# Kernel optimization log

Measured on AMD Instinct MI355X. Metric: run time of the kernel, lower is better.

## Reference

```python
import jax, jax.numpy as jnp
import numpy as np

VOCAB, SEQ, D_IN, HID, N_CLS, BATCH = 50257, 128, 768, 512, 9, 256


def setup_inputs() -> dict:
    key = jax.random.key(0)
    ks = jax.random.split(key, 12)
    s = 0.02
    return {
        "input_ids": jax.random.randint(ks[0], (BATCH, SEQ), 0, VOCAB),
        "tok_emb": jax.random.normal(ks[1], (VOCAB, D_IN), jnp.float32) * s,
        "pos_emb": jax.random.normal(ks[2], (SEQ, D_IN), jnp.float32) * s,
        # stacked per-gate Linear weights, gate order (i, f, g, o); Linear stores (out, in)
        "W1": jax.random.normal(ks[3], (4, HID, D_IN), jnp.float32) * s,
        "R1": jax.random.normal(ks[4], (4, HID, HID), jnp.float32) * s,
        "b1": jax.random.normal(ks[5], (4, HID), jnp.float32) * s,
        "W2": jax.random.normal(ks[6], (4, HID, HID), jnp.float32) * s,
        "R2": jax.random.normal(ks[7], (4, HID, HID), jnp.float32) * s,
        "b2": jax.random.normal(ks[8], (4, HID), jnp.float32) * s,
        "Wo": jax.random.normal(ks[9], (N_CLS, HID), jnp.float32) * s,
        "bo": jax.random.normal(ks[10], (N_CLS,), jnp.float32) * s,
    }


def _cell(x, h, c, W, R, b):
    # all four gate linears fused into one einsum each for x and h
    g = jnp.einsum('bi,ghi->gbh', x, W) + jnp.einsum('bj,ghj->gbh', h, R) + b[:, None, :]
    i = jax.nn.sigmoid(g[0])
    f = jax.nn.sigmoid(g[1])
    m = jnp.tanh(g[2])
    o = jax.nn.sigmoid(g[3])
    c_next = m * i + f * c
    h_next = o * jnp.tanh(c_next)
    return h_next, c_next


def reference(input_ids, tok_emb, pos_emb, W1, R1, b1, W2, R2, b2, Wo, bo):
    embeds = tok_emb[input_ids] + pos_emb[None, :, :]  # (B, S, D)
    B = embeds.shape[0]
    H = R1.shape[-1]
    x_seq = jnp.swapaxes(embeds, 0, 1)  # (S, B, D)
    init = tuple(jnp.zeros((B, H), embeds.dtype) for _ in range(4))

    def step(carry, x_t):
        h1, c1, h2, c2 = carry
        h1, c1 = _cell(x_t, h1, c1, W1, R1, b1)
        h2, c2 = _cell(h1, h2, c2, W2, R2, b2)
        out = h2 @ Wo.T + bo  # (B, num_class)
        return (h1, c1, h2, c2), out

    _, outs = jax.lax.scan(step, init, x_seq)  # (S, B, C)
    return jnp.swapaxes(outs, 0, 1)  # (B, S, C)
```

## Files before the change

kernel.cpp:

```cpp
#include <hip/hip_runtime.h>
#include <hip/hip_bf16.h>
#include <stdint.h>

#define BATCH_ 256
#define SEQ_   128
#define DIN_   768
#define HID_   512
#define NG_    2048
#define NCLS_  9

typedef unsigned short u16;
typedef unsigned int u32;
typedef unsigned long long u64;
typedef __attribute__((ext_vector_type(8))) short bf16x8;
typedef __attribute__((ext_vector_type(4))) float f32x4;

__device__ __forceinline__ float bf2f(u16 u) {
  return __builtin_bit_cast(float, (uint32_t)u << 16);
}
__device__ __forceinline__ u16 f2bf(float f) {
  uint32_t x = __builtin_bit_cast(uint32_t, f);
  uint32_t r = (x + 0x7fffu + ((x >> 16) & 1u)) >> 16;
  return (u16)r;
}

__device__ __forceinline__ void gload_lds16(const void* g, void* l) {
#if defined(__has_builtin)
#if __has_builtin(__builtin_amdgcn_global_load_lds)
  __builtin_amdgcn_global_load_lds((const __attribute__((address_space(1))) void*)g,
                                   (__attribute__((address_space(3))) void*)l, 16, 0, 0);
  return;
#endif
#endif
  *(uint4*)l = *(const uint4*)g;
}

__device__ __forceinline__ u32 aload32(const u32* p) {
  return __hip_atomic_load(p, __ATOMIC_RELAXED, __HIP_MEMORY_SCOPE_AGENT);
}
__device__ __forceinline__ void astore32(u32* p, u32 v) {
  __hip_atomic_store(p, v, __ATOMIC_RELAXED, __HIP_MEMORY_SCOPE_AGENT);
}

__global__ void castk(const float* __restrict__ s, u16* __restrict__ d, int n4) {
  int i = blockIdx.x * blockDim.x + threadIdx.x;
  if (i < n4) {
    float4 v = ((const float4*)s)[i];
    ushort4 o;
    o.x = f2bf(v.x); o.y = f2bf(v.y); o.z = f2bf(v.z); o.w = f2bf(v.w);
    ((ushort4*)d)[i] = o;
  }
}

__global__ __launch_bounds__(192) void embed_k(const int* __restrict__ ids,
                                               const float* __restrict__ tok,
                                               const float* __restrict__ pos,
                                               u16* __restrict__ X) {
  const int row = blockIdx.x;
  const int t = row >> 8, b = row & 255;
  const int id = ids[b * SEQ_ + t];
  const float4* tr = (const float4*)(tok + (size_t)id * DIN_);
  const float4* pr = (const float4*)(pos + (size_t)t * DIN_);
  const int i = threadIdx.x;
  float4 v = tr[i], p = pr[i];
  ushort4 o;
  o.x = f2bf(v.x + p.x); o.y = f2bf(v.y + p.y);
  o.z = f2bf(v.z + p.z); o.w = f2bf(v.w + p.w);
  ((ushort4*)(X + (size_t)row * DIN_))[i] = o;
}

__global__ __launch_bounds__(256) void gemm_bt(const u16* __restrict__ A,
                                               const u16* __restrict__ Bm,
                                               const float* __restrict__ bias,
                                               u16* __restrict__ C,
                                               int M, int N, int K) {
  __shared__ __align__(16) u16 As[128 * 64];
  __shared__ __align__(16) u16 Bs[128 * 64];
  const int tid = threadIdx.x;
  const int lane = tid & 63;
  const int wave = tid >> 6;
  const int m0 = blockIdx.y * 128;
  const int n0 = blockIdx.x * 128;
  const int wm = (wave >> 1) * 64;
  const int wn = (wave & 1) * 64;
  const int lr = lane & 15;
  const int lg = lane >> 4;
  f32x4 acc[4][4] = {};

  for (int k0 = 0; k0 < K; k0 += 64) {
#pragma unroll
    for (int it = 0; it < 4; ++it) {
      int e = it * 256 + tid;
      int r = e >> 3, c8 = (e & 7) * 8;
      gload_lds16(A + (size_t)(m0 + r) * K + k0 + c8, &As[e * 8]);
      gload_lds16(Bm + (size_t)(n0 + r) * K + k0 + c8, &Bs[e * 8]);
    }
    __syncthreads();
#pragma unroll
    for (int kk = 0; kk < 64; kk += 32) {
      bf16x8 af[4], bfr[4];
#pragma unroll
      for (int i = 0; i < 4; ++i) {
        af[i]  = *(const bf16x8*)&As[(wm + i * 16 + lr) * 64 + kk + lg * 8];
        bfr[i] = *(const bf16x8*)&Bs[(wn + i * 16 + lr) * 64 + kk + lg * 8];
      }
#pragma unroll
      for (int i = 0; i < 4; ++i)
#pragma unroll
        for (int j = 0; j < 4; ++j)
          acc[i][j] = __builtin_amdgcn_mfma_f32_16x16x32_bf16(af[i], bfr[j], acc[i][j], 0, 0, 0);
    }
    __syncthreads();
  }
#pragma unroll
  for (int i = 0; i < 4; ++i) {
#pragma unroll
    for (int j = 0; j < 4; ++j) {
      int col = n0 + wn + j * 16 + lr;
      float bv = bias[col];
#pragma unroll
      for (int q = 0; q < 4; ++q) {
        int row = m0 + wm + i * 16 + lg * 4 + q;
        C[(size_t)row * N + col] = f2bf(acc[i][j][q] + bv);
      }
    }
  }
}

__device__ __forceinline__ void stage32r(char* dst, const u16* src, int tid) {
  const u64* s64 = (const u64*)src;
#pragma unroll
  for (int i = 0; i < 8; ++i) {
    int e = i * 512 + tid, r = e >> 7, c8 = e & 127;
    u64 v = s64[(size_t)r * 128 + c8];
    *(u64*)(dst + r * 1024 + ((((c8 >> 1) ^ (r & 7)) << 4) | ((c8 & 1) << 3))) = v;
  }
}

__global__ __launch_bounds__(512, 2) void lstm_duo3(
    const u16* __restrict__ Xpre,
    u16* __restrict__ H1,
    u16* __restrict__ H2,
    const u16* __restrict__ R1b,
    const u16* __restrict__ W2b,
    const u16* __restrict__ R2b,
    const float* __restrict__ b2,
    u32* __restrict__ cnt1, u32* __restrict__ cnt2) {
  __shared__ __align__(16) char As1[32 * 1024];
  __shared__ __align__(16) char As2[32 * 1024];
  __shared__ float Gsf[2 * 4 * 32 * 33];
  const int tid = threadIdx.x;
  const int lane = tid & 63;
  const int w = tid >> 6;
  const int lr = lane & 15, lg = lane >> 4;
  const int kind = blockIdx.x >> 7;
  const int lb = blockIdx.x & 127;
  const int m8 = lb & 7, j16 = lb >> 3;
  const int m0 = m8 * 32, j0 = j16 * 32;
  const int g = w & 3, kh = w >> 2;
  const int cr = tid >> 4, cc = (tid & 15) * 2;
#define GS(KH, GG, RR, CC) Gsf[(((KH) * 4 + (GG)) * 32 + (RR)) * 33 + (CC)]

  if (kind == 0) {
    bf16x8 B1[2][8];
#pragma unroll
    for (int nf = 0; nf < 2; ++nf)
#pragma unroll
      for (int k = 0; k < 8; ++k)
        B1[nf][k] = *(const bf16x8*)&R1b[(size_t)(g * 512 + j0 + nf * 16 + lr) * 512 +
                                         kh * 256 + k * 32 + lg * 8];
    float cst0 = 0.f, cst1 = 0.f;

    for (int t = 0; t < SEQ_; ++t) {
      u32 xp[4];
#pragma unroll
      for (int gg = 0; gg < 4; ++gg)
        xp[gg] = *(const u32*)(Xpre + (size_t)t * (BATCH_ * NG_) +
                               (size_t)(m0 + cr) * NG_ + gg * 512 + j0 + cc);
      if (t > 0) {
        if (w == 0 && lane == 0) {
          const u32* f = cnt1 + (size_t)(t - 1) * 8 + m8;
          int spins = 0;
          while (aload32(f) < 16u) {
            __builtin_amdgcn_s_sleep(1);
            if (++spins > (1 << 21)) break;
          }
        }
        __syncthreads();
        stage32r(As1, H1 + ((size_t)(t - 1) * BATCH_ + m0) * HID_, tid);
      }
      __syncthreads();
      f32x4 acc[2][2] = {};
      if (t > 0) {
#pragma unroll
        for (int k = 0; k < 8; ++k) {
          int c = kh * 32 + k * 4 + lg;
          int sw = ((c ^ (lr & 7)) << 4);
          bf16x8 a0 = *(const bf16x8*)(As1 + (lr) * 1024 + sw);
          bf16x8 a1 = *(const bf16x8*)(As1 + (16 + lr) * 1024 + sw);
          acc[0][0] = __builtin_amdgcn_mfma_f32_16x16x32_bf16(a0, B1[0][k], acc[0][0], 0, 0, 0);
          acc[0][1] = __builtin_amdgcn_mfma_f32_16x16x32_bf16(a0, B1[1][k], acc[0][1], 0, 0, 0);
          acc[1][0] = __builtin_amdgcn_mfma_f32_16x16x32_bf16(a1, B1[0][k], acc[1][0], 0, 0, 0);
          acc[1][1] = __builtin_amdgcn_mfma_f32_16x16x32_bf16(a1, B1[1][k], acc[1][1], 0, 0, 0);
        }
      }
#pragma unroll
      for (int mf = 0; mf < 2; ++mf)
#pragma unroll
        for (int nf = 0; nf < 2; ++nf)
#pragma unroll
          for (int q = 0; q < 4; ++q)
            GS(kh, g, mf * 16 + lg * 4 + q, nf * 16 + lr) = acc[mf][nf][q];
      __syncthreads();
      {
        float G[4][2];
#pragma unroll
        for (int gg = 0; gg < 4; ++gg) {
          G[gg][0] = GS(0, gg, cr, cc) + GS(1, gg, cr, cc) + bf2f((u16)xp[gg]);
          G[gg][1] = GS(0, gg, cr, cc + 1) + GS(1, gg, cr, cc + 1) + bf2f((u16)(xp[gg] >> 16));
        }
        u32 pack = 0;
        {
          float iv = 1.f / (1.f + expf(-G[0][0]));
          float fv = 1.f / (1.f + expf(-G[1][0]));
          float mv = tanhf(G[2][0]);
          float ov = 1.f / (1.f + expf(-G[3][0]));
          float cn = mv * iv + fv * cst0; cst0 = cn;
          pack |= (u32)f2bf(ov * tanhf(cn));
        }
        {
          float iv = 1.f / (1.f + expf(-G[0][1]));
          float fv = 1.f / (1.f + expf(-G[1][1]));
          float mv = tanhf(G[2][1]);
          float ov = 1.f / (1.f + expf(-G[3][1]));
          float cn = mv * iv + fv * cst1; cst1 = cn;
          pack |= (u32)f2bf(ov * tanhf(cn)) << 16;
        }
        astore32((u32*)(H1 + (size_t)t * (BATCH_ * HID_) +
                        (size_t)(m0 + cr) * HID_ + j0 + cc), pack);
      }
      __syncthreads();
      if (tid == 0)
        __hip_atomic_fetch_add(cnt1 + (size_t)t * 8 + m8, 1u,
                               __ATOMIC_RELAXED, __HIP_MEMORY_SCOPE_AGENT);
    }
  } else {
    const u16* Bmat = kh ? R2b : W2b;
    bf16x8 Bw[2][16];
#pragma unroll
    for (int nf = 0; nf < 2; ++nf)
#pragma unroll
      for (int k = 0; k < 16; ++k)
        Bw[nf][k] = *(const bf16x8*)&Bmat[(size_t)(g * 512 + j0 + nf * 16 + lr) * 512 +
                                          k * 32 + lg * 8];
    float bc[4][2];
#pragma unroll
    for (int gg = 0; gg < 4; ++gg) {
      bc[gg][0] = b2[gg * 512 + j0 + cc];
      bc[gg][1] = b2[gg * 512 + j0 + cc + 1];
    }
    float cst0 = 0.f, cst1 = 0.f;

    for (int t = 0; t < SEQ_; ++t) {
      if (w == 0) {
        const u32* fa = cnt1 + (size_t)t * 8 + m8;
        const u32* fb = cnt2 + (size_t)(t > 0 ? t - 1 : 0) * 8 + m8;
        int spins = 0;
        while (true) {
          bool ok = true;
          if (lane == 0) ok = aload32(fa) >= 16u;
          else if (lane == 1) ok = (t == 0) || (aload32(fb) >= 16u);
          if (__all(ok)) break;
          __builtin_amdgcn_s_sleep(1);
          if (++spins > (1 << 21)) break;
        }
      }
      __syncthreads();
      stage32r(As1, H1 + ((size_t)t * BATCH_ + m0) * HID_, tid);
      if (t > 0)
        stage32r(As2, H2 + ((size_t)(t - 1) * BATCH_ + m0) * HID_, tid);
      __syncthreads();
      f32x4 acc[2][2] = {};
      if (kh == 0 || t > 0) {
        const char* As = kh ? As2 : As1;
#pragma unroll
        for (int k = 0; k < 16; ++k) {
          int c = k * 4 + lg;
          int sw = ((c ^ (lr & 7)) << 4);
          bf16x8 a0 = *(const bf16x8*)(As + (lr) * 1024 + sw);
          bf16x8 a1 = *(const bf16x8*)(As + (16 + lr) * 1024 + sw);
          acc[0][0] = __builtin_amdgcn_mfma_f32_16x16x32_bf16(a0, Bw[0][k], acc[0][0], 0, 0, 0);
          acc[0][1] = __builtin_amdgcn_mfma_f32_16x16x32_bf16(a0, Bw[1][k], acc[0][1], 0, 0, 0);
          acc[1][0] = __builtin_amdgcn_mfma_f32_16x16x32_bf16(a1, Bw[0][k], acc[1][0], 0, 0, 0);
          acc[1][1] = __builtin_amdgcn_mfma_f32_16x16x32_bf16(a1, Bw[1][k], acc[1][1], 0, 0, 0);
        }
      }
#pragma unroll
      for (int mf = 0; mf < 2; ++mf)
#pragma unroll
        for (int nf = 0; nf < 2; ++nf)
#pragma unroll
          for (int q = 0; q < 4; ++q)
            GS(kh, g, mf * 16 + lg * 4 + q, nf * 16 + lr) = acc[mf][nf][q];
      __syncthreads();
      {
        float G[4][2];
#pragma unroll
        for (int gg = 0; gg < 4; ++gg) {
          G[gg][0] = GS(0, gg, cr, cc) + GS(1, gg, cr, cc) + bc[gg][0];
          G[gg][1] = GS(0, gg, cr, cc + 1) + GS(1, gg, cr, cc + 1) + bc[gg][1];
        }
        u32 pack = 0;
        {
          float iv = 1.f / (1.f + expf(-G[0][0]));
          float fv = 1.f / (1.f + expf(-G[1][0]));
          float mv = tanhf(G[2][0]);
          float ov = 1.f / (1.f + expf(-G[3][0]));
          float cn = mv * iv + fv * cst0; cst0 = cn;
          pack |= (u32)f2bf(ov * tanhf(cn));
        }
        {
          float iv = 1.f / (1.f + expf(-G[0][1]));
          float fv = 1.f / (1.f + expf(-G[1][1]));
          float mv = tanhf(G[2][1]);
          float ov = 1.f / (1.f + expf(-G[3][1]));
          float cn = mv * iv + fv * cst1; cst1 = cn;
          pack |= (u32)f2bf(ov * tanhf(cn)) << 16;
        }
        astore32((u32*)(H2 + (size_t)t * (BATCH_ * HID_) +
                        (size_t)(m0 + cr) * HID_ + j0 + cc), pack);
      }
      __syncthreads();
      if (tid == 0)
        __hip_atomic_fetch_add(cnt2 + (size_t)t * 8 + m8, 1u,
                               __ATOMIC_RELAXED, __HIP_MEMORY_SCOPE_AGENT);
    }
  }
#undef GS
}

__global__ __launch_bounds__(320) void out_proj(const u16* __restrict__ H2,
                                                const float* __restrict__ Wo,
                                                const float* __restrict__ bo,
                                                float* __restrict__ out) {
  __shared__ __align__(16) u16 Hs[32 * 520];
  const int r0 = blockIdx.x * 32;
  const int tid = threadIdx.x;
  for (int e = tid; e < 2048; e += 320) {
    int rl = e >> 6, k8 = (e & 63) * 8;
    *(uint4*)&Hs[rl * 520 + k8] = *(const uint4*)(H2 + (size_t)(r0 + rl) * HID_ + k8);
  }
  __syncthreads();
  if (tid < 288) {
    int rl = tid / 9, cls = tid - rl * 9;
    const u16* h = &Hs[rl * 520];
    const float* wv = Wo + cls * HID_;
    float s = bo[cls];
#pragma unroll 8
    for (int k = 0; k < HID_; ++k) s += bf2f(h[k]) * wv[k];
    int r = r0 + rl, t = r >> 8, b = r & 255;
    out[((size_t)b * SEQ_ + t) * NCLS_ + cls] = s;
  }
}

extern "C" void kernel_launch(void* const* d_in, const int* in_sizes, int n_in,
                              void* d_out, int out_size, void* d_ws, size_t ws_size,
                              hipStream_t stream) {
  (void)in_sizes; (void)n_in; (void)out_size; (void)ws_size;
  const int*   ids = (const int*)d_in[0];
  const float* tok = (const float*)d_in[1];
  const float* pos = (const float*)d_in[2];
  const float* W1  = (const float*)d_in[3];
  const float* R1  = (const float*)d_in[4];
  const float* b1  = (const float*)d_in[5];
  const float* W2  = (const float*)d_in[6];
  const float* R2  = (const float*)d_in[7];
  const float* b2  = (const float*)d_in[8];
  const float* Wo  = (const float*)d_in[9];
  const float* bo  = (const float*)d_in[10];
  float* out = (float*)d_out;

  char* p = (char*)d_ws;
  auto alloc = [&](size_t bytes) { char* q = p; p += (bytes + 255) & ~(size_t)255; return q; };
  u16*  W1b  = (u16*)alloc((size_t)NG_ * DIN_ * 2);
  u16*  R1b  = (u16*)alloc((size_t)NG_ * HID_ * 2);
  u16*  W2b  = (u16*)alloc((size_t)NG_ * HID_ * 2);
  u16*  R2b  = (u16*)alloc((size_t)NG_ * HID_ * 2);
  u32*  cnt1 = (u32*)alloc((size_t)SEQ_ * 8 * 4);
  u32*  cnt2 = (u32*)alloc((size_t)SEQ_ * 8 * 4);
  size_t xbf_bytes = (size_t)SEQ_ * BATCH_ * DIN_ * 2;
  u16*  Xbf  = (u16*)alloc(xbf_bytes);
  u16*  H1all = Xbf;
  u16*  H2all = (u16*)alloc((size_t)SEQ_ * BATCH_ * HID_ * 2);
  u16*  Xpre = (u16*)alloc((size_t)SEQ_ * BATCH_ * NG_ * 2);

  castk<<<dim3((NG_ * DIN_ / 4 + 255) / 256), 256, 0, stream>>>(W1, W1b, NG_ * DIN_ / 4);
  castk<<<dim3((NG_ * HID_ / 4 + 255) / 256), 256, 0, stream>>>(R1, R1b, NG_ * HID_ / 4);
  castk<<<dim3((NG_ * HID_ / 4 + 255) / 256), 256, 0, stream>>>(W2, W2b, NG_ * HID_ / 4);
  castk<<<dim3((NG_ * HID_ / 4 + 255) / 256), 256, 0, stream>>>(R2, R2b, NG_ * HID_ / 4);
  hipMemsetAsync(cnt1, 0, (size_t)2 * SEQ_ * 8 * 4, stream);

  embed_k<<<dim3(SEQ_ * BATCH_), 192, 0, stream>>>(ids, tok, pos, Xbf);

  gemm_bt<<<dim3(NG_ / 128, SEQ_ * BATCH_ / 128), 256, 0, stream>>>(
      Xbf, W1b, b1, Xpre, SEQ_ * BATCH_, NG_, DIN_);

  {
    const u16* Xp = Xpre; u16* H1a = H1all; u16* H2a = H2all;
    const u16* R1a = R1b; const u16* W2a = W2b; const u16* R2a = R2b;
    const float* b2a = b2;
    u32* c1 = cnt1; u32* c2 = cnt2;
    void* args[] = {(void*)&Xp, (void*)&H1a, (void*)&H2a, (void*)&R1a,
                    (void*)&W2a, (void*)&R2a, (void*)&b2a, (void*)&c1, (void*)&c2};
    hipLaunchCooperativeKernel(reinterpret_cast<void*>(&lstm_duo3),
                               dim3(256), dim3(512), args, 0, stream);
  }

  out_proj<<<dim3(SEQ_ * BATCH_ / 32), 320, 0, stream>>>(H2all, Wo, bo, out);
}
```

Before: 913.1 us.

## Fuse layer-1 input projection into the persistent LSTM kernel

Drops the separate bf16 GEMM that precomputed X·W1ᵀ for all timesteps. Each layer-1 block now keeps its slice of W1 in registers, stages the embedding rows for each step into LDS, and computes the input projection before it waits on the step flag, so that work overlaps the wait on the recurrence. This removes the large Xpre write and read plus a kernel launch. In exchange it adds register pressure from 24 more bf16x8 fragments and a larger LDS footprint of about 113KB, which could hurt occupancy or cause spills given the 2-blocks-per-CU launch bound.

Result: slower. 1.212 ms (+32.7%).

```diff
diff --git a/kernel.cpp b/kernel.cpp
--- a/kernel.cpp
+++ b/kernel.cpp
@@ -22,17 +22,6 @@
   uint32_t x = __builtin_bit_cast(uint32_t, f);
   uint32_t r = (x + 0x7fffu + ((x >> 16) & 1u)) >> 16;
   return (u16)r;
-}
-
-__device__ __forceinline__ void gload_lds16(const void* g, void* l) {
-#if defined(__has_builtin)
-#if __has_builtin(__builtin_amdgcn_global_load_lds)
-  __builtin_amdgcn_global_load_lds((const __attribute__((address_space(1))) void*)g,
-                                   (__attribute__((address_space(3))) void*)l, 16, 0, 0);
-  return;
-#endif
-#endif
-  *(uint4*)l = *(const uint4*)g;
 }
 
 __device__ __forceinline__ u32 aload32(const u32* p) {
@@ -69,64 +58,6 @@
   ((ushort4*)(X + (size_t)row * DIN_))[i] = o;
 }
 
-__global__ __launch_bounds__(256) void gemm_bt(const u16* __restrict__ A,
-                                               const u16* __restrict__ Bm,
-                                               const float* __restrict__ bias,
-                                               u16* __restrict__ C,
-                                               int M, int N, int K) {
-  __shared__ __align__(16) u16 As[128 * 64];
-  __shared__ __align__(16) u16 Bs[128 * 64];
-  const int tid = threadIdx.x;
-  const int lane = tid & 63;
-  const int wave = tid >> 6;
-  const int m0 = blockIdx.y * 128;
-  const int n0 = blockIdx.x * 128;
-  const int wm = (wave >> 1) * 64;
-  const int wn = (wave & 1) * 64;
-  const int lr = lane & 15;
-  const int lg = lane >> 4;
-  f32x4 acc[4][4] = {};
-
-  for (int k0 = 0; k0 < K; k0 += 64) {
-#pragma unroll
-    for (int it = 0; it < 4; ++it) {
-      int e = it * 256 + tid;
-      int r = e >> 3, c8 = (e & 7) * 8;
-      gload_lds16(A + (size_t)(m0 + r) * K + k0 + c8, &As[e * 8]);
-      gload_lds16(Bm + (size_t)(n0 + r) * K + k0 + c8, &Bs[e * 8]);
-    }
-    __syncthreads();
-#pragma unroll
-    for (int kk = 0; kk < 64; kk += 32) {
-      bf16x8 af[4], bfr[4];
-#pragma unroll
-      for (int i = 0; i < 4; ++i) {
-        af[i]  = *(const bf16x8*)&As[(wm + i * 16 + lr) * 64 + kk + lg * 8];
-        bfr[i] = *(const bf16x8*)&Bs[(wn + i * 16 + lr) * 64 + kk + lg * 8];
-      }
-#pragma unroll
-      for (int i = 0; i < 4; ++i)
-#pragma unroll
-        for (int j = 0; j < 4; ++j)
-          acc[i][j] = __builtin_amdgcn_mfma_f32_16x16x32_bf16(af[i], bfr[j], acc[i][j], 0, 0, 0);
-    }
-    __syncthreads();
-  }
-#pragma unroll
-  for (int i = 0; i < 4; ++i) {
-#pragma unroll
-    for (int j = 0; j < 4; ++j) {
-      int col = n0 + wn + j * 16 + lr;
-      float bv = bias[col];
-#pragma unroll
-      for (int q = 0; q < 4; ++q) {
-        int row = m0 + wm + i * 16 + lg * 4 + q;
-        C[(size_t)row * N + col] = f2bf(acc[i][j][q] + bv);
-      }
-    }
-  }
-}
-
 __device__ __forceinline__ void stage32r(char* dst, const u16* src, int tid) {
   const u64* s64 = (const u64*)src;
 #pragma unroll
@@ -137,18 +68,30 @@
   }
 }
 
-__global__ __launch_bounds__(512, 2) void lstm_duo3(
-    const u16* __restrict__ Xpre,
+__device__ __forceinline__ void stage32x(char* dst, const u16* src, int tid) {
+  const u64* s64 = (const u64*)src;
+#pragma unroll
+  for (int i = 0; i < 12; ++i) {
+    int e = i * 512 + tid;
+    int r = e / 192, c8 = e - r * 192;
+    u64 v = s64[(size_t)r * 192 + c8];
+    int c16 = c8 >> 1, lo = c8 & 1;
+    *(u64*)(dst + r * 1536 + (((c16 ^ (r & 7)) << 4) | (lo << 3))) = v;
+  }
+}
+
+__global__ __launch_bounds__(512, 2) void lstm_duo4(
+    const u16* __restrict__ Xemb,
     u16* __restrict__ H1,
     u16* __restrict__ H2,
+    const u16* __restrict__ W1b,
     const u16* __restrict__ R1b,
     const u16* __restrict__ W2b,
     const u16* __restrict__ R2b,
+    const float* __restrict__ b1,
     const float* __restrict__ b2,
     u32* __restrict__ cnt1, u32* __restrict__ cnt2) {
-  __shared__ __align__(16) char As1[32 * 1024];
-  __shared__ __align__(16) char As2[32 * 1024];
-  __shared__ float Gsf[2 * 4 * 32 * 33];
+  __shared__ __align__(16) char lds[115712];
   const int tid = threadIdx.x;
   const int lane = tid & 63;
   const int w = tid >> 6;
@@ -159,9 +102,19 @@
   const int m0 = m8 * 32, j0 = j16 * 32;
   const int g = w & 3, kh = w >> 2;
   const int cr = tid >> 4, cc = (tid & 15) * 2;
+  float* Gsf = (float*)(lds + 81920);
 #define GS(KH, GG, RR, CC) Gsf[(((KH) * 4 + (GG)) * 32 + (RR)) * 33 + (CC)]
 
   if (kind == 0) {
+    char* Xs = lds;
+    char* Ash = lds + 49152;
+    bf16x8 Wx[2][12];
+#pragma unroll
+    for (int nf = 0; nf < 2; ++nf)
+#pragma unroll
+      for (int k = 0; k < 12; ++k)
+        Wx[nf][k] = *(const bf16x8*)&W1b[(size_t)(g * 512 + j0 + nf * 16 + lr) * 768 +
+                                         kh * 384 + k * 32 + lg * 8];
     bf16x8 B1[2][8];
 #pragma unroll
     for (int nf = 0; nf < 2; ++nf)
@@ -169,35 +122,49 @@
       for (int k = 0; k < 8; ++k)
         B1[nf][k] = *(const bf16x8*)&R1b[(size_t)(g * 512 + j0 + nf * 16 + lr) * 512 +
                                          kh * 256 + k * 32 + lg * 8];
+    float bc[4][2];
+#pragma unroll
+    for (int gg = 0; gg < 4; ++gg) {
+      bc[gg][0] = b1[gg * 512 + j0 + cc];
+      bc[gg][1] = b1[gg * 512 + j0 + cc + 1];
+    }
     float cst0 = 0.f, cst1 = 0.f;
 
     for (int t = 0; t < SEQ_; ++t) {
-      u32 xp[4];
-#pragma unroll
-      for (int gg = 0; gg < 4; ++gg)
-        xp[gg] = *(const u32*)(Xpre + (size_t)t * (BATCH_ * NG_) +
-                               (size_t)(m0 + cr) * NG_ + gg * 512 + j0 + cc);
+      stage32x(Xs, Xemb + ((size_t)t * BATCH_ + m0) * DIN_, tid);
+      __syncthreads();
+      f32x4 acc[2][2] = {};
+#pragma unroll
+      for (int k = 0; k < 12; ++k) {
+        int c = kh * 48 + k * 4 + lg;
+        int sw = ((c ^ (lr & 7)) << 4);
+        bf16x8 a0 = *(const bf16x8*)(Xs + lr * 1536 + sw);
+        bf16x8 a1 = *(const bf16x8*)(Xs + (16 + lr) * 1536 + sw);
+        acc[0][0] = __builtin_amdgcn_mfma_f32_16x16x32_bf16(a0, Wx[0][k], acc[0][0], 0, 0, 0);
+        acc[0][1] = __builtin_amdgcn_mfma_f32_16x16x32_bf16(a0, Wx[1][k], acc[0][1], 0, 0, 0);
+        acc[1][0] = __builtin_amdgcn_mfma_f32_16x16x32_bf16(a1, Wx[0][k], acc[1][0], 0, 0, 0);
+        acc[1][1] = __builtin_amdgcn_mfma_f32_16x16x32_bf16(a1, Wx[1][k], acc[1][1], 0, 0, 0);
+      }
+      if (t > 0 && w == 0 && lane == 0) {
+        const u32* f = cnt1 + (size_t)(t - 1) * 8 + m8;
+        int spins = 0;
+        while (aload32(f) < 16u) {
+          __builtin_amdgcn_s_sleep(1);
+          if (++spins > (1 << 21)) break;
+        }
+      }
+      __syncthreads();
       if (t > 0) {
-        if (w == 0 && lane == 0) {
-          const u32* f = cnt1 + (size_t)(t - 1) * 8 + m8;
-          int spins = 0;
-          while (aload32(f) < 16u) {
-            __builtin_amdgcn_s_sleep(1);
-            if (++spins > (1 << 21)) break;
-          }
-        }
-        __syncthreads();
-        stage32r(As1, H1 + ((size_t)(t - 1) * BATCH_ + m0) * HID_, tid);
-      }
-      __syncthreads();
-      f32x4 acc[2][2] = {};
+        stage32r(Ash, H1 + ((size_t)(t - 1) * BATCH_ + m0) * HID_, tid);
+      }
+      __syncthreads();
       if (t > 0) {
 #pragma unroll
         for (int k = 0; k < 8; ++k) {
           int c = kh * 32 + k * 4 + lg;
           int sw = ((c ^ (lr & 7)) << 4);
-          bf16x8 a0 = *(const bf16x8*)(As1 + (lr) * 1024 + sw);
-          bf16x8 a1 = *(const bf16x8*)(As1 + (16 + lr) * 1024 + sw);
+          bf16x8 a0 = *(const bf16x8*)(Ash + lr * 1024 + sw);
+          bf16x8 a1 = *(const bf16x8*)(Ash + (16 + lr) * 1024 + sw);
           acc[0][0] = __builtin_amdgcn_mfma_f32_16x16x32_bf16(a0, B1[0][k], acc[0][0], 0, 0, 0);
           acc[0][1] = __builtin_amdgcn_mfma_f32_16x16x32_bf16(a0, B1[1][k], acc[0][1], 0, 0, 0);
           acc[1][0] = __builtin_amdgcn_mfma_f32_16x16x32_bf16(a1, B1[0][k], acc[1][0], 0, 0, 0);
@@ -216,8 +183,8 @@
         float G[4][2];
 #pragma unroll
         for (int gg = 0; gg < 4; ++gg) {
-          G[gg][0] = GS(0, gg, cr, cc) + GS(1, gg, cr, cc) + bf2f((u16)xp[gg]);
-          G[gg][1] = GS(0, gg, cr, cc + 1) + GS(1, gg, cr, cc + 1) + bf2f((u16)(xp[gg] >> 16));
+          G[gg][0] = GS(0, gg, cr, cc) + GS(1, gg, cr, cc) + bc[gg][0];
+          G[gg][1] = GS(0, gg, cr, cc + 1) + GS(1, gg, cr, cc + 1) + bc[gg][1];
         }
         u32 pack = 0;
         {
@@ -245,6 +212,8 @@
                                __ATOMIC_RELAXED, __HIP_MEMORY_SCOPE_AGENT);
     }
   } else {
+    char* As1 = lds;
+    char* As2 = lds + 32768;
     const u16* Bmat = kh ? R2b : W2b;
     bf16x8 Bw[2][16];
 #pragma unroll
@@ -388,11 +357,9 @@
   u16*  R2b  = (u16*)alloc((size_t)NG_ * HID_ * 2);
   u32*  cnt1 = (u32*)alloc((size_t)SEQ_ * 8 * 4);
   u32*  cnt2 = (u32*)alloc((size_t)SEQ_ * 8 * 4);
-  size_t xbf_bytes = (size_t)SEQ_ * BATCH_ * DIN_ * 2;
-  u16*  Xbf  = (u16*)alloc(xbf_bytes);
-  u16*  H1all = Xbf;
+  u16*  Xemb = (u16*)alloc((size_t)SEQ_ * BATCH_ * DIN_ * 2);
+  u16*  H1all = (u16*)alloc((size_t)SEQ_ * BATCH_ * HID_ * 2);
   u16*  H2all = (u16*)alloc((size_t)SEQ_ * BATCH_ * HID_ * 2);
-  u16*  Xpre = (u16*)alloc((size_t)SEQ_ * BATCH_ * NG_ * 2);
 
   castk<<<dim3((NG_ * DIN_ / 4 + 255) / 256), 256, 0, stream>>>(W1, W1b, NG_ * DIN_ / 4);
   castk<<<dim3((NG_ * HID_ / 4 + 255) / 256), 256, 0, stream>>>(R1, R1b, NG_ * HID_ / 4);
@@ -400,19 +367,18 @@
   castk<<<dim3((NG_ * HID_ / 4 + 255) / 256), 256, 0, stream>>>(R2, R2b, NG_ * HID_ / 4);
   hipMemsetAsync(cnt1, 0, (size_t)2 * SEQ_ * 8 * 4, stream);
 
-  embed_k<<<dim3(SEQ_ * BATCH_), 192, 0, stream>>>(ids, tok, pos, Xbf);
-
-  gemm_bt<<<dim3(NG_ / 128, SEQ_ * BATCH_ / 128), 256, 0, stream>>>(
-      Xbf, W1b, b1, Xpre, SEQ_ * BATCH_, NG_, DIN_);
+  embed_k<<<dim3(SEQ_ * BATCH_), 192, 0, stream>>>(ids, tok, pos, Xemb);
 
   {
-    const u16* Xp = Xpre; u16* H1a = H1all; u16* H2a = H2all;
-    const u16* R1a = R1b; const u16* W2a = W2b; const u16* R2a = R2b;
-    const float* b2a = b2;
+    const u16* Xp = Xemb; u16* H1a = H1all; u16* H2a = H2all;
+    const u16* W1a = W1b; const u16* R1a = R1b;
+    const u16* W2a = W2b; const u16* R2a = R2b;
+    const float* b1a = b1; const float* b2a = b2;
     u32* c1 = cnt1; u32* c2 = cnt2;
-    void* args[] = {(void*)&Xp, (void*)&H1a, (void*)&H2a, (void*)&R1a,
-                    (void*)&W2a, (void*)&R2a, (void*)&b2a, (void*)&c1, (void*)&c2};
-    hipLaunchCooperativeKernel(reinterpret_cast<void*>(&lstm_duo3),
+    void* args[] = {(void*)&Xp, (void*)&H1a, (void*)&H2a, (void*)&W1a, (void*)&R1a,
+                    (void*)&W2a, (void*)&R2a, (void*)&b1a, (void*)&b2a,
+                    (void*)&c1, (void*)&c2};
+    hipLaunchCooperativeKernel(reinterpret_cast<void*>(&lstm_duo4),
                                dim3(256), dim3(512), args, 0, stream);
   }
 
```
